# Kernel optimization log

Measured on AMD Instinct MI355X. Metric: run time of the kernel, lower is better.

The kernel has to match this reference:

```python
import jax, jax.numpy as jnp
import numpy as np

N = 100000           # nodes
E = 1600000          # directed edges (avg degree 16)
G = 64               # graphs in batch


def gcn_conv(x, src, dst, ew, W, b, n):
    """PyG GCNConv with edge weights and self-loops already appended.

    out[i] = sum_{(j->i)} d[j]^-1/2 * ew * d[i]^-1/2 * (x W)[j] + b
    where d[i] = sum of incoming edge weights at i (incl. self-loop).
    """
    xw = x @ W                                               # [n, out]
    deg = jax.ops.segment_sum(ew, dst, num_segments=n)       # [n]
    dinv = jnp.where(deg > 0, jax.lax.rsqrt(deg), 0.0)
    norm = dinv[src] * ew * dinv[dst]                        # [e]
    msg = xw[src] * norm[:, None]                            # [e, out] gather
    out = jax.ops.segment_sum(msg, dst, num_segments=n)      # scatter-add
    return out + b


def setup_inputs() -> dict:
    key = jax.random.key(0)
    ks = jax.random.split(key, 10)
    x = jax.random.normal(ks[0], (N, 256), dtype=jnp.float32)
    edge_index = jax.random.randint(ks[1], (2, E), 0, N, dtype=jnp.int64)
    edge_weight = jax.random.uniform(ks[2], (E,), dtype=jnp.float32)
    batch = jnp.sort(jax.random.randint(ks[3], (N,), 0, G, dtype=jnp.int64))
    s = 0.05
    W1 = jax.random.normal(ks[4], (256, 128), dtype=jnp.float32) * s
    b1 = jnp.zeros((128,), dtype=jnp.float32)
    W2 = jax.random.normal(ks[5], (128, 64), dtype=jnp.float32) * s
    b2 = jnp.zeros((64,), dtype=jnp.float32)
    Wfc = jax.random.normal(ks[6], (64, 1), dtype=jnp.float32) * s
    bfc = jnp.zeros((1,), dtype=jnp.float32)
    return {"x": x, "edge_index": edge_index, "edge_weight": edge_weight,
            "batch": batch, "W1": W1, "b1": b1, "W2": W2, "b2": b2,
            "Wfc": Wfc, "bfc": bfc}


def reference(x, edge_index, edge_weight, batch, W1, b1, W2, b2, Wfc, bfc):
    n = x.shape[0]
    loop = jnp.arange(n, dtype=edge_index.dtype)
    src = jnp.concatenate([edge_index[0], loop])             # add self-loops
    dst = jnp.concatenate([edge_index[1], loop])
    ew = jnp.concatenate([edge_weight, jnp.ones((n,), x.dtype)])

    h = jax.nn.relu(gcn_conv(x, src, dst, ew, W1, b1, n))    # [N,128]
    h = jax.nn.relu(gcn_conv(h, src, dst, ew, W2, b2, n))    # [N,64]

    # global_mean_pool over batch ids
    sums = jax.ops.segment_sum(h, batch, num_segments=G)     # [G,64]
    cnt = jax.ops.segment_sum(jnp.ones((n,), h.dtype), batch, num_segments=G)
    pooled = sums / jnp.maximum(cnt, 1.0)[:, None]
    return pooled @ Wfc + bfc                                # [G,1]
```

## Files before the change

kernel.cpp:

```cpp
#include <hip/hip_runtime.h>
#include <hip/hip_bf16.h>
#include <hip/hip_fp16.h>
#include <hip/hip_fp8.h>


static inline int ceil_div_ll(long long a, int b) { return (int)((a + b - 1) / b); }

typedef __attribute__((ext_vector_type(8))) short bf16x8;
typedef __attribute__((ext_vector_type(4))) float f32x4;

#define FIX_SCALE 33554432.0f

__device__ inline unsigned short f2bf(float f) {
    __hip_bfloat16 h = __float2bfloat16(f);
    return *reinterpret_cast<unsigned short*>(&h);
}
__device__ inline float bf2f(unsigned short u) {
    unsigned int x = ((unsigned int)u) << 16;
    return __uint_as_float(x);
}
__device__ inline unsigned char f32_to_fp8(float f) {
    return __hip_cvt_float_to_fp8(f, __HIP_SATFINITE, __HIP_E4M3);
}
__device__ inline float fp8_to_f32(unsigned int v) {
    unsigned int s = v >> 7;
    unsigned int e = (v >> 3) & 15;
    unsigned int m = v & 7;
    float r;
    if (e) r = __uint_as_float(((e + 120) << 23) | (m << 20));
    else   r = (float)m * 0.001953125f;
    return s ? -r : r;
}

__global__ void k_init_pk(unsigned long long* __restrict__ pk, int n) {
    int i = blockIdx.x * blockDim.x + threadIdx.x;
    if (i < n) pk[i] = (unsigned long long)(1u << 25);
}

__global__ void k_deg_count(const int* __restrict__ dst, const float* __restrict__ ew,
                            unsigned long long* __restrict__ pk, int* __restrict__ slot, int E) {
    int t = blockIdx.x * blockDim.x + threadIdx.x;
    int e = t * 4;
    if (e + 4 <= E) {
        int4   d4 = *(const int4*)(dst + e);
        float4 w4 = *(const float4*)(ew + e);
        unsigned long long o0 = atomicAdd(&pk[d4.x],
            (1ull << 32) | (unsigned long long)__float2uint_rn(w4.x * FIX_SCALE));
        unsigned long long o1 = atomicAdd(&pk[d4.y],
            (1ull << 32) | (unsigned long long)__float2uint_rn(w4.y * FIX_SCALE));
        unsigned long long o2 = atomicAdd(&pk[d4.z],
            (1ull << 32) | (unsigned long long)__float2uint_rn(w4.z * FIX_SCALE));
        unsigned long long o3 = atomicAdd(&pk[d4.w],
            (1ull << 32) | (unsigned long long)__float2uint_rn(w4.w * FIX_SCALE));
        *(int4*)(slot + e) = make_int4((int)(o0 >> 32), (int)(o1 >> 32),
                                       (int)(o2 >> 32), (int)(o3 >> 32));
    } else if (e < E) {
        for (int k = e; k < E; ++k) {
            unsigned int fx = __float2uint_rn(ew[k] * FIX_SCALE);
            unsigned long long old =
                atomicAdd(&pk[dst[k]], (1ull << 32) | (unsigned long long)fx);
            slot[k] = (int)(old >> 32);
        }
    }
}

__global__ void k_finish(const unsigned long long* __restrict__ pk, float* __restrict__ dinv,
                         int* __restrict__ count, float* __restrict__ sums, int nsums, int n) {
    int i = blockIdx.x * blockDim.x + threadIdx.x;
    if (i < n) {
        unsigned long long v = pk[i];
        float deg = (float)(unsigned int)(v & 0xffffffffull) * (1.0f / FIX_SCALE);
        dinv[i] = (deg > 0.f) ? rsqrtf(deg) : 0.f;
        count[i] = (int)(v >> 32);
    }
    if (i < nsums) sums[i] = 0.0f;
}

constexpr int SC_T = 256;
constexpr int SC_PER = 16;
constexpr int SC_CHUNK = SC_T * SC_PER;

__global__ void k_scan_a(const int* __restrict__ count, int* __restrict__ bsum, int n) {
    __shared__ int lds[SC_T];
    int b = blockIdx.x, t = threadIdx.x;
    int base = b * SC_CHUNK + t * SC_PER;
    int s = 0;
#pragma unroll
    for (int k = 0; k < SC_PER; ++k) {
        int idx = base + k;
        if (idx < n) s += count[idx];
    }
    lds[t] = s;
    __syncthreads();
    for (int off = 128; off > 0; off >>= 1) {
        if (t < off) lds[t] += lds[t + off];
        __syncthreads();
    }
    if (t == 0) bsum[b] = lds[0];
}

__global__ void k_scan_b(int* __restrict__ bsum, int nb) {
    if (threadIdx.x == 0) {
        int run = 0;
        for (int i = 0; i < nb; ++i) { int c = bsum[i]; bsum[i] = run; run += c; }
    }
}

__global__ void k_scan_c(const int* __restrict__ count, int* __restrict__ rowptr,
                         const int* __restrict__ bsum, int n) {
    __shared__ int lds[SC_T];
    int b = blockIdx.x, t = threadIdx.x;
    int base = b * SC_CHUNK + t * SC_PER;
    int v[SC_PER];
    int s = 0;
#pragma unroll
    for (int k = 0; k < SC_PER; ++k) {
        int idx = base + k;
        v[k] = (idx < n) ? count[idx] : 0;
        s += v[k];
    }
    lds[t] = s;
    for (int off = 1; off < SC_T; off <<= 1) {
        __syncthreads();
        int tmp = (t >= off) ? lds[t - off] : 0;
        __syncthreads();
        lds[t] += tmp;
    }
    __syncthreads();
    int run = bsum[b] + lds[t] - s;
#pragma unroll
    for (int k = 0; k < SC_PER; ++k) {
        int idx = base + k;
        if (idx < n) {
            rowptr[idx] = run;
            run += v[k];
            if (idx == n - 1) rowptr[n] = run;
        }
    }
}

__global__ void k_csr_fill(const int* __restrict__ src, const int* __restrict__ dst,
                           const float* __restrict__ ew, const float* __restrict__ dinv,
                           const int* __restrict__ rowptr, const int* __restrict__ slot,
                           int2* __restrict__ csr, int E) {
    int e = blockIdx.x * blockDim.x + threadIdx.x;
    if (e < E) {
        int s = src[e], d = dst[e];
        int pos = rowptr[d] + slot[e];
        float coef = dinv[s] * ew[e] * dinv[d];
        csr[pos] = make_int2(s, __float_as_int(coef));
    }
}

template <int KDIM, int ODIM>
__global__ void k_wpack(const float* __restrict__ W, unsigned short* __restrict__ wpk) {
    constexpr int NKS = KDIM / 32, NF = ODIM / 16;
    int t = blockIdx.x * blockDim.x + threadIdx.x;
    if (t >= NKS * NF * 64) return;
    int lane = t & 63;
    int nf   = (t >> 6) % NF;
    int ks   = t / (64 * NF);
    int col  = nf * 16 + (lane & 15);
    int kb   = ks * 32 + (lane >> 4) * 8;
    bf16x8 hi, lo;
#pragma unroll
    for (int i = 0; i < 8; ++i) {
        float w = W[(size_t)(kb + i) * ODIM + col];
        unsigned short h = f2bf(w);
        hi[i] = (short)h;
        lo[i] = (short)f2bf(w - bf2f(h));
    }
    size_t base = (size_t)t * 8;
    *(bf16x8*)(wpk + base) = hi;
    *(bf16x8*)(wpk + (size_t)KDIM * ODIM + base) = lo;
}

template <int KDIM, int ODIM>
__global__ void k_gemm_mfma(const float* __restrict__ X,
                            const unsigned short* __restrict__ wpk,
                            unsigned char* __restrict__ Y, int n) {
    constexpr int NKS = KDIM / 32, NF = ODIM / 16;
    int wid  = threadIdx.x >> 6;
    int lane = threadIdx.x & 63;
    int rowbase = blockIdx.x * 64 + wid * 16;
    int arow = rowbase + (lane & 15);
    int kb0  = (lane >> 4) * 8;
    const unsigned short* wlo = wpk + (size_t)KDIM * ODIM;
    bool aok = (arow < n);
    const float* xr = X + (size_t)arow * KDIM + kb0;

    f32x4 acc[NF];
#pragma unroll
    for (int f = 0; f < NF; ++f) acc[f] = (f32x4){0.f, 0.f, 0.f, 0.f};

#pragma unroll
    for (int ks = 0; ks < NKS; ++ks) {
        f32x4 a0 = (f32x4){0.f, 0.f, 0.f, 0.f};
        f32x4 a1 = (f32x4){0.f, 0.f, 0.f, 0.f};
        if (aok) {
            a0 = *(const f32x4*)(xr + ks * 32);
            a1 = *(const f32x4*)(xr + ks * 32 + 4);
        }
        bf16x8 ahi, alo;
#pragma unroll
        for (int i = 0; i < 4; ++i) {
            unsigned short h0 = f2bf(a0[i]);
            ahi[i]     = (short)h0;
            alo[i]     = (short)f2bf(a0[i] - bf2f(h0));
            unsigned short h1 = f2bf(a1[i]);
            ahi[i + 4] = (short)h1;
            alo[i + 4] = (short)f2bf(a1[i] - bf2f(h1));
        }
#pragma unroll
        for (int f = 0; f < NF; ++f) {
            size_t fb = (((size_t)ks * NF + f) * 64 + lane) * 8;
            bf16x8 bhi = *(const bf16x8*)(wpk + fb);
            bf16x8 blo = *(const bf16x8*)(wlo + fb);
            acc[f] = __builtin_amdgcn_mfma_f32_16x16x32_bf16(ahi, bhi, acc[f], 0, 0, 0);
            acc[f] = __builtin_amdgcn_mfma_f32_16x16x32_bf16(alo, bhi, acc[f], 0, 0, 0);
            acc[f] = __builtin_amdgcn_mfma_f32_16x16x32_bf16(ahi, blo, acc[f], 0, 0, 0);
        }
    }

    int r0  = rowbase + (lane >> 4) * 4;
    int col = lane & 15;
#pragma unroll
    for (int f = 0; f < NF; ++f) {
#pragma unroll
        for (int i = 0; i < 4; ++i) {
            int r = r0 + i;
            if (r < n) Y[(size_t)r * ODIM + f * 16 + col] = f32_to_fp8(acc[f][i]);
        }
    }
}

template <int KDIM, int ODIM>
__global__ void k_gemm_mfma_bfA(const unsigned short* __restrict__ X,
                                const unsigned short* __restrict__ wpk,
                                unsigned short* __restrict__ Y, int n) {
    constexpr int NKS = KDIM / 32, NF = ODIM / 16;
    int wid  = threadIdx.x >> 6;
    int lane = threadIdx.x & 63;
    int rowbase = blockIdx.x * 64 + wid * 16;
    int arow = rowbase + (lane & 15);
    int kb0  = (lane >> 4) * 8;
    const unsigned short* wlo = wpk + (size_t)KDIM * ODIM;
    bool aok = (arow < n);
    const unsigned short* xr = X + (size_t)arow * KDIM + kb0;

    f32x4 acc[NF];
#pragma unroll
    for (int f = 0; f < NF; ++f) acc[f] = (f32x4){0.f, 0.f, 0.f, 0.f};

#pragma unroll
    for (int ks = 0; ks < NKS; ++ks) {
        bf16x8 a = (bf16x8){0, 0, 0, 0, 0, 0, 0, 0};
        if (aok) a = *(const bf16x8*)(xr + ks * 32);
#pragma unroll
        for (int f = 0; f < NF; ++f) {
            size_t fb = (((size_t)ks * NF + f) * 64 + lane) * 8;
            bf16x8 bhi = *(const bf16x8*)(wpk + fb);
            bf16x8 blo = *(const bf16x8*)(wlo + fb);
            acc[f] = __builtin_amdgcn_mfma_f32_16x16x32_bf16(a, bhi, acc[f], 0, 0, 0);
            acc[f] = __builtin_amdgcn_mfma_f32_16x16x32_bf16(a, blo, acc[f], 0, 0, 0);
        }
    }

    int r0  = rowbase + (lane >> 4) * 4;
    int col = lane & 15;
#pragma unroll
    for (int f = 0; f < NF; ++f) {
#pragma unroll
        for (int i = 0; i < 4; ++i) {
            int r = r0 + i;
            if (r < n) Y[(size_t)r * ODIM + f * 16 + col] = f2bf(acc[f][i]);
        }
    }
}

__global__ __launch_bounds__(256, 2)
void k_gather1(const unsigned char* __restrict__ xw, const int* __restrict__ rowptr,
               const int2* __restrict__ csr,
               const float* __restrict__ dinv, const float* __restrict__ bias,
               unsigned short* __restrict__ out, int n) {
    int wave = threadIdx.x >> 6;
    int lane = threadIdx.x & 63;
    int i = blockIdx.x * 4 + wave;
    if (i >= n) return;

    float dv = dinv[i];
    float sl = dv * dv;
    int e0 = __builtin_amdgcn_readfirstlane(rowptr[i]);
    int e1 = __builtin_amdgcn_readfirstlane(rowptr[i + 1]);

    const unsigned short* base = (const unsigned short*)xw;
    unsigned int su = base[(size_t)i * 64 + lane];
    float ax0 = fp8_to_f32(su & 0xff) * sl;
    float ay0 = fp8_to_f32(su >> 8) * sl;
    float ax1 = 0.f, ay1 = 0.f, ax2 = 0.f, ay2 = 0.f, ax3 = 0.f, ay3 = 0.f;
    int e = e0;
    for (; e + 8 <= e1; e += 8) {
        int2 p0 = csr[e + 0], p1 = csr[e + 1], p2 = csr[e + 2], p3 = csr[e + 3];
        int2 p4 = csr[e + 4], p5 = csr[e + 5], p6 = csr[e + 6], p7 = csr[e + 7];
        unsigned int u0 = base[(size_t)p0.x * 64 + lane];
        unsigned int u1 = base[(size_t)p1.x * 64 + lane];
        unsigned int u2 = base[(size_t)p2.x * 64 + lane];
        unsigned int u3 = base[(size_t)p3.x * 64 + lane];
        unsigned int u4 = base[(size_t)p4.x * 64 + lane];
        unsigned int u5 = base[(size_t)p5.x * 64 + lane];
        unsigned int u6 = base[(size_t)p6.x * 64 + lane];
        unsigned int u7 = base[(size_t)p7.x * 64 + lane];
        float c0 = __int_as_float(p0.y), c1 = __int_as_float(p1.y);
        float c2 = __int_as_float(p2.y), c3 = __int_as_float(p3.y);
        float c4 = __int_as_float(p4.y), c5 = __int_as_float(p5.y);
        float c6 = __int_as_float(p6.y), c7 = __int_as_float(p7.y);
        ax0 += c0 * fp8_to_f32(u0 & 0xff); ay0 += c0 * fp8_to_f32(u0 >> 8);
        ax1 += c1 * fp8_to_f32(u1 & 0xff); ay1 += c1 * fp8_to_f32(u1 >> 8);
        ax2 += c2 * fp8_to_f32(u2 & 0xff); ay2 += c2 * fp8_to_f32(u2 >> 8);
        ax3 += c3 * fp8_to_f32(u3 & 0xff); ay3 += c3 * fp8_to_f32(u3 >> 8);
        ax0 += c4 * fp8_to_f32(u4 & 0xff); ay0 += c4 * fp8_to_f32(u4 >> 8);
        ax1 += c5 * fp8_to_f32(u5 & 0xff); ay1 += c5 * fp8_to_f32(u5 >> 8);
        ax2 += c6 * fp8_to_f32(u6 & 0xff); ay2 += c6 * fp8_to_f32(u6 >> 8);
        ax3 += c7 * fp8_to_f32(u7 & 0xff); ay3 += c7 * fp8_to_f32(u7 >> 8);
    }
    for (; e + 2 <= e1; e += 2) {
        int2 p0 = csr[e + 0], p1 = csr[e + 1];
        unsigned int u0 = base[(size_t)p0.x * 64 + lane];
        unsigned int u1 = base[(size_t)p1.x * 64 + lane];
        float c0 = __int_as_float(p0.y), c1 = __int_as_float(p1.y);
        ax0 += c0 * fp8_to_f32(u0 & 0xff); ay0 += c0 * fp8_to_f32(u0 >> 8);
        ax1 += c1 * fp8_to_f32(u1 & 0xff); ay1 += c1 * fp8_to_f32(u1 >> 8);
    }
    if (e < e1) {
        int2 p0 = csr[e];
        unsigned int u0 = base[(size_t)p0.x * 64 + lane];
        float c0 = __int_as_float(p0.y);
        ax0 += c0 * fp8_to_f32(u0 & 0xff); ay0 += c0 * fp8_to_f32(u0 >> 8);
    }
    float2 bb = *((const float2*)bias + lane);
    float rx = fmaxf((ax0 + ax1) + (ax2 + ax3) + bb.x, 0.f);
    float ry = fmaxf((ay0 + ay1) + (ay2 + ay3) + bb.y, 0.f);
    unsigned int packed = (unsigned int)f2bf(rx) | ((unsigned int)f2bf(ry) << 16);
    ((unsigned int*)(out + (size_t)i * 128))[lane] = packed;
}

__global__ __launch_bounds__(256, 2)
void k_gather2_pool(const unsigned short* __restrict__ xw, const int* __restrict__ rowptr,
                    const int2* __restrict__ csr,
                    const float* __restrict__ dinv, const float* __restrict__ bias,
                    const int* __restrict__ batch, float* __restrict__ sums, int n) {
    constexpr int NPW = 4;
    int gwave = (blockIdx.x * blockDim.x + threadIdx.x) >> 6;
    int lane = threadIdx.x & 63;
    int i0 = gwave * NPW;
    if (i0 >= n) return;
    int i1 = min(i0 + NPW, n);

    float bb = bias[lane];
    float acc = 0.f;
    int cg = __builtin_amdgcn_readfirstlane(batch[i0]);

    for (int i = i0; i < i1; ++i) {
        int g = __builtin_amdgcn_readfirstlane(batch[i]);
        if (g != cg) {
            atomicAdd(&sums[cg * 64 + lane], acc);
            acc = 0.f;
            cg = g;
        }
        float dv = dinv[i];
        float sl = dv * dv;
        int e0 = __builtin_amdgcn_readfirstlane(rowptr[i]);
        int e1 = __builtin_amdgcn_readfirstlane(rowptr[i + 1]);

        float a0 = bf2f(xw[(size_t)i * 64 + lane]) * sl;
        float a1 = 0.f, a2 = 0.f, a3 = 0.f;
        int e = e0;
        for (; e + 8 <= e1; e += 8) {
            int2 p0 = csr[e + 0], p1 = csr[e + 1], p2 = csr[e + 2], p3 = csr[e + 3];
            int2 p4 = csr[e + 4], p5 = csr[e + 5], p6 = csr[e + 6], p7 = csr[e + 7];
            float v0 = bf2f(xw[(size_t)p0.x * 64 + lane]);
            float v1 = bf2f(xw[(size_t)p1.x * 64 + lane]);
            float v2 = bf2f(xw[(size_t)p2.x * 64 + lane]);
            float v3 = bf2f(xw[(size_t)p3.x * 64 + lane]);
            float v4 = bf2f(xw[(size_t)p4.x * 64 + lane]);
            float v5 = bf2f(xw[(size_t)p5.x * 64 + lane]);
            float v6 = bf2f(xw[(size_t)p6.x * 64 + lane]);
            float v7 = bf2f(xw[(size_t)p7.x * 64 + lane]);
            a0 += __int_as_float(p0.y) * v0; a1 += __int_as_float(p1.y) * v1;
            a2 += __int_as_float(p2.y) * v2; a3 += __int_as_float(p3.y) * v3;
            a0 += __int_as_float(p4.y) * v4; a1 += __int_as_float(p5.y) * v5;
            a2 += __int_as_float(p6.y) * v6; a3 += __int_as_float(p7.y) * v7;
        }
        for (; e + 2 <= e1; e += 2) {
            int2 p0 = csr[e + 0], p1 = csr[e + 1];
            a0 += __int_as_float(p0.y) * bf2f(xw[(size_t)p0.x * 64 + lane]);
            a1 += __int_as_float(p1.y) * bf2f(xw[(size_t)p1.x * 64 + lane]);
        }
        if (e < e1) {
            int2 p0 = csr[e];
            a0 += __int_as_float(p0.y) * bf2f(xw[(size_t)p0.x * 64 + lane]);
        }
        acc += fmaxf((a0 + a1) + (a2 + a3) + bb, 0.f);
    }
    atomicAdd(&sums[cg * 64 + lane], acc);
}

__global__ void k_head(const float* __restrict__ sums, const int* __restrict__ batch,
                       const float* __restrict__ Wfc, const float* __restrict__ bfc,
                       float* __restrict__ out, int n) {
    int g = blockIdx.x;
    int f = threadIdx.x;
    int lo0 = 0, hi0 = n;
    while (lo0 < hi0) { int m = (lo0 + hi0) >> 1; if (batch[m] < g) lo0 = m + 1; else hi0 = m; }
    int lo1 = lo0, hi1 = n;
    while (lo1 < hi1) { int m = (lo1 + hi1) >> 1; if (batch[m] < g + 1) lo1 = m + 1; else hi1 = m; }
    float cnt = (float)(lo1 - lo0);
    float v = sums[g * 64 + f] * Wfc[f];
#pragma unroll
    for (int o = 32; o > 0; o >>= 1) v += __shfl_down(v, o);
    if (f == 0) out[g] = v / fmaxf(cnt, 1.0f) + bfc[0];
}

extern "C" void kernel_launch(void* const* d_in, const int* in_sizes, int n_in,
                              void* d_out, int out_size, void* d_ws, size_t ws_size,
                              hipStream_t stream) {
    const float* x    = (const float*)d_in[0];
    const int*   ei   = (const int*)d_in[1];
    const float* ew   = (const float*)d_in[2];
    const int*   bat  = (const int*)d_in[3];
    const float* W1   = (const float*)d_in[4];
    const float* b1   = (const float*)d_in[5];
    const float* W2   = (const float*)d_in[6];
    const float* b2   = (const float*)d_in[7];
    const float* Wfc  = (const float*)d_in[8];
    const float* bfc  = (const float*)d_in[9];
    float*       out  = (float*)d_out;

    const int N = in_sizes[0] / 256;
    const int E = in_sizes[2];
    const int G = out_size;

    const int* src = ei;
    const int* dst = ei + E;

    const int NB_SCAN = (N + SC_CHUNK - 1) / SC_CHUNK;

    const int Npad = (N + 4) & ~3;
    unsigned long long* pk     = (unsigned long long*)d_ws;
    float*              dinv   = (float*)(pk + Npad);
    int*                count  = (int*)(dinv + Npad);
    int*                rowptr = count + Npad;
    int*                bsum   = rowptr + Npad;
    int*                slot   = bsum + ((NB_SCAN + 4) & ~3);
    int2*               csr    = (int2*)(slot + ((E + 4) & ~3));
    unsigned short*     wpk1   = (unsigned short*)(csr + E);
    unsigned short*     wpk2   = wpk1 + 2 * 256 * 128;
    float*              sums   = (float*)(wpk2 + 2 * 128 * 64);
    unsigned char*      bufA   = (unsigned char*)(sums + ((G * 64 + 4) & ~3));
    unsigned short*     bufH1  = (unsigned short*)(bufA + (size_t)N * 128);

    const int B = 256;

    k_init_pk<<<ceil_div_ll(N, B), B, 0, stream>>>(pk, N);
    k_deg_count<<<ceil_div_ll((E + 3) / 4, B), B, 0, stream>>>(dst, ew, pk, slot, E);
    k_finish<<<ceil_div_ll(N, B), B, 0, stream>>>(pk, dinv, count, sums, G * 64, N);

    k_scan_a<<<NB_SCAN, SC_T, 0, stream>>>(count, bsum, N);
    k_scan_b<<<1, 64, 0, stream>>>(bsum, NB_SCAN);
    k_scan_c<<<NB_SCAN, SC_T, 0, stream>>>(count, rowptr, bsum, N);
    k_csr_fill<<<ceil_div_ll(E, B), B, 0, stream>>>(src, dst, ew, dinv, rowptr,
                                                    slot, csr, E);

    k_wpack<256, 128><<<(8 * 8 * 64 + B - 1) / B, B, 0, stream>>>(W1, wpk1);
    k_wpack<128, 64><<<(4 * 4 * 64 + B - 1) / B, B, 0, stream>>>(W2, wpk2);

    k_gemm_mfma<256, 128><<<ceil_div_ll(N, 64), 256, 0, stream>>>(x, wpk1, bufA, N);
    k_gather1<<<ceil_div_ll(N, 4), 256, 0, stream>>>(
        bufA, rowptr, csr, dinv, b1, bufH1, N);

    k_gemm_mfma_bfA<128, 64><<<ceil_div_ll(N, 64), 256, 0, stream>>>(
        bufH1, wpk2, (unsigned short*)bufA, N);
    {
        int waves = ceil_div_ll(N, 4);
        int blocks = ceil_div_ll(waves, 4);
        k_gather2_pool<<<blocks, 256, 0, stream>>>(
            (const unsigned short*)bufA, rowptr, csr, dinv, b2, bat, sums, N);
    }

    k_head<<<G, 64, 0, stream>>>(sums, bat, Wfc, bfc, out, N);
}
```

Measured before the change: 359.2 us.

## Split each wave into two half-waves gathering different edges with wider loads

Both gather kernels now have each half of a 64-lane wave handle alternate edges. Each lane loads 4 bytes per neighbor row instead of 2, so one wave-wide load fetches two neighbor rows. The halves' partial sums are combined with a cross-half shuffle before bias, ReLU and output. This is meant to issue fewer, wider memory instructions per edge. The cost is extra shuffles, extra select logic for the odd-edge tail, and more per-lane conversion work.

```diff
diff --git a/kernel.cpp b/kernel.cpp
--- a/kernel.cpp
+++ b/kernel.cpp
@@ -15,9 +15,8 @@
     __hip_bfloat16 h = __float2bfloat16(f);
     return *reinterpret_cast<unsigned short*>(&h);
 }
-__device__ inline float bf2f(unsigned short u) {
-    unsigned int x = ((unsigned int)u) << 16;
-    return __uint_as_float(x);
+__device__ inline float bf2f(unsigned int u) {
+    return __uint_as_float((u & 0xffffu) << 16);
 }
 __device__ inline unsigned char f32_to_fp8(float f) {
     return __hip_cvt_float_to_fp8(f, __HIP_SATFINITE, __HIP_E4M3);
@@ -285,6 +284,8 @@
                unsigned short* __restrict__ out, int n) {
     int wave = threadIdx.x >> 6;
     int lane = threadIdx.x & 63;
+    int half = lane >> 5;
+    int hl   = lane & 31;
     int i = blockIdx.x * 4 + wave;
     if (i >= n) return;
 
@@ -293,55 +294,60 @@
     int e0 = __builtin_amdgcn_readfirstlane(rowptr[i]);
     int e1 = __builtin_amdgcn_readfirstlane(rowptr[i + 1]);
 
-    const unsigned short* base = (const unsigned short*)xw;
-    unsigned int su = base[(size_t)i * 64 + lane];
-    float ax0 = fp8_to_f32(su & 0xff) * sl;
-    float ay0 = fp8_to_f32(su >> 8) * sl;
-    float ax1 = 0.f, ay1 = 0.f, ax2 = 0.f, ay2 = 0.f, ax3 = 0.f, ay3 = 0.f;
+    unsigned int su = *(const unsigned int*)(xw + (size_t)i * 128 + hl * 4);
+    float s0 = fp8_to_f32(su & 0xff) * sl;
+    float s1 = fp8_to_f32((su >> 8) & 0xff) * sl;
+    float s2 = fp8_to_f32((su >> 16) & 0xff) * sl;
+    float s3 = fp8_to_f32(su >> 24) * sl;
+
+    float ac0 = 0.f, ac1 = 0.f, ac2 = 0.f, ac3 = 0.f;
     int e = e0;
     for (; e + 8 <= e1; e += 8) {
-        int2 p0 = csr[e + 0], p1 = csr[e + 1], p2 = csr[e + 2], p3 = csr[e + 3];
-        int2 p4 = csr[e + 4], p5 = csr[e + 5], p6 = csr[e + 6], p7 = csr[e + 7];
-        unsigned int u0 = base[(size_t)p0.x * 64 + lane];
-        unsigned int u1 = base[(size_t)p1.x * 64 + lane];
-        unsigned int u2 = base[(size_t)p2.x * 64 + lane];
-        unsigned int u3 = base[(size_t)p3.x * 64 + lane];
-        unsigned int u4 = base[(size_t)p4.x * 64 + lane];
-        unsigned int u5 = base[(size_t)p5.x * 64 + lane];
-        unsigned int u6 = base[(size_t)p6.x * 64 + lane];
-        unsigned int u7 = base[(size_t)p7.x * 64 + lane];
-        float c0 = __int_as_float(p0.y), c1 = __int_as_float(p1.y);
-        float c2 = __int_as_float(p2.y), c3 = __int_as_float(p3.y);
-        float c4 = __int_as_float(p4.y), c5 = __int_as_float(p5.y);
-        float c6 = __int_as_float(p6.y), c7 = __int_as_float(p7.y);
-        ax0 += c0 * fp8_to_f32(u0 & 0xff); ay0 += c0 * fp8_to_f32(u0 >> 8);
-        ax1 += c1 * fp8_to_f32(u1 & 0xff); ay1 += c1 * fp8_to_f32(u1 >> 8);
-        ax2 += c2 * fp8_to_f32(u2 & 0xff); ay2 += c2 * fp8_to_f32(u2 >> 8);
-        ax3 += c3 * fp8_to_f32(u3 & 0xff); ay3 += c3 * fp8_to_f32(u3 >> 8);
-        ax0 += c4 * fp8_to_f32(u4 & 0xff); ay0 += c4 * fp8_to_f32(u4 >> 8);
-        ax1 += c5 * fp8_to_f32(u5 & 0xff); ay1 += c5 * fp8_to_f32(u5 >> 8);
-        ax2 += c6 * fp8_to_f32(u6 & 0xff); ay2 += c6 * fp8_to_f32(u6 >> 8);
-        ax3 += c7 * fp8_to_f32(u7 & 0xff); ay3 += c7 * fp8_to_f32(u7 >> 8);
+        int2 q0 = csr[e + 0 + half];
+        int2 q1 = csr[e + 2 + half];
+        int2 q2 = csr[e + 4 + half];
+        int2 q3 = csr[e + 6 + half];
+        unsigned int u0 = *(const unsigned int*)(xw + (size_t)q0.x * 128 + hl * 4);
+        unsigned int u1 = *(const unsigned int*)(xw + (size_t)q1.x * 128 + hl * 4);
+        unsigned int u2 = *(const unsigned int*)(xw + (size_t)q2.x * 128 + hl * 4);
+        unsigned int u3 = *(const unsigned int*)(xw + (size_t)q3.x * 128 + hl * 4);
+        float c0 = __int_as_float(q0.y), c1 = __int_as_float(q1.y);
+        float c2 = __int_as_float(q2.y), c3 = __int_as_float(q3.y);
+        ac0 += c0 * fp8_to_f32(u0 & 0xff);         ac1 += c0 * fp8_to_f32((u0 >> 8) & 0xff);
+        ac2 += c0 * fp8_to_f32((u0 >> 16) & 0xff); ac3 += c0 * fp8_to_f32(u0 >> 24);
+        ac0 += c1 * fp8_to_f32(u1 & 0xff);         ac1 += c1 * fp8_to_f32((u1 >> 8) & 0xff);
+        ac2 += c1 * fp8_to_f32((u1 >> 16) & 0xff); ac3 += c1 * fp8_to_f32(u1 >> 24);
+        ac0 += c2 * fp8_to_f32(u2 & 0xff);         ac1 += c2 * fp8_to_f32((u2 >> 8) & 0xff);
+        ac2 += c2 * fp8_to_f32((u2 >> 16) & 0xff); ac3 += c2 * fp8_to_f32(u2 >> 24);
+        ac0 += c3 * fp8_to_f32(u3 & 0xff);         ac1 += c3 * fp8_to_f32((u3 >> 8) & 0xff);
+        ac2 += c3 * fp8_to_f32((u3 >> 16) & 0xff); ac3 += c3 * fp8_to_f32(u3 >> 24);
     }
     for (; e + 2 <= e1; e += 2) {
-        int2 p0 = csr[e + 0], p1 = csr[e + 1];
-        unsigned int u0 = base[(size_t)p0.x * 64 + lane];
-        unsigned int u1 = base[(size_t)p1.x * 64 + lane];
-        float c0 = __int_as_float(p0.y), c1 = __int_as_float(p1.y);
-        ax0 += c0 * fp8_to_f32(u0 & 0xff); ay0 += c0 * fp8_to_f32(u0 >> 8);
-        ax1 += c1 * fp8_to_f32(u1 & 0xff); ay1 += c1 * fp8_to_f32(u1 >> 8);
+        int2 q = csr[e + half];
+        unsigned int u = *(const unsigned int*)(xw + (size_t)q.x * 128 + hl * 4);
+        float c = __int_as_float(q.y);
+        ac0 += c * fp8_to_f32(u & 0xff);         ac1 += c * fp8_to_f32((u >> 8) & 0xff);
+        ac2 += c * fp8_to_f32((u >> 16) & 0xff); ac3 += c * fp8_to_f32(u >> 24);
     }
     if (e < e1) {
-        int2 p0 = csr[e];
-        unsigned int u0 = base[(size_t)p0.x * 64 + lane];
-        float c0 = __int_as_float(p0.y);
-        ax0 += c0 * fp8_to_f32(u0 & 0xff); ay0 += c0 * fp8_to_f32(u0 >> 8);
-    }
-    float2 bb = *((const float2*)bias + lane);
-    float rx = fmaxf((ax0 + ax1) + (ax2 + ax3) + bb.x, 0.f);
-    float ry = fmaxf((ay0 + ay1) + (ay2 + ay3) + bb.y, 0.f);
-    unsigned int packed = (unsigned int)f2bf(rx) | ((unsigned int)f2bf(ry) << 16);
-    ((unsigned int*)(out + (size_t)i * 128))[lane] = packed;
+        int2 q = csr[e];
+        unsigned int u = *(const unsigned int*)(xw + (size_t)q.x * 128 + hl * 4);
+        float c = half ? 0.f : __int_as_float(q.y);
+        ac0 += c * fp8_to_f32(u & 0xff);         ac1 += c * fp8_to_f32((u >> 8) & 0xff);
+        ac2 += c * fp8_to_f32((u >> 16) & 0xff); ac3 += c * fp8_to_f32(u >> 24);
+    }
+    ac0 += __shfl_xor(ac0, 32);
+    ac1 += __shfl_xor(ac1, 32);
+    ac2 += __shfl_xor(ac2, 32);
+    ac3 += __shfl_xor(ac3, 32);
+    float4 bb = ((const float4*)bias)[hl];
+    float f0 = fmaxf(ac0 + s0 + bb.x, 0.f);
+    float f1 = fmaxf(ac1 + s1 + bb.y, 0.f);
+    float f2 = fmaxf(ac2 + s2 + bb.z, 0.f);
+    float f3 = fmaxf(ac3 + s3 + bb.w, 0.f);
+    unsigned int w = half ? ((unsigned int)f2bf(f2) | ((unsigned int)f2bf(f3) << 16))
+                          : ((unsigned int)f2bf(f0) | ((unsigned int)f2bf(f1) << 16));
+    ((unsigned int*)(out + (size_t)i * 128))[2 * hl + half] = w;
 }
 
 __global__ __launch_bounds__(256, 2)
@@ -352,19 +358,22 @@
     constexpr int NPW = 4;
     int gwave = (blockIdx.x * blockDim.x + threadIdx.x) >> 6;
     int lane = threadIdx.x & 63;
+    int half = lane >> 5;
+    int hl   = lane & 31;
     int i0 = gwave * NPW;
     if (i0 >= n) return;
     int i1 = min(i0 + NPW, n);
 
-    float bb = bias[lane];
-    float acc = 0.f;
+    float2 bb = ((const float2*)bias)[hl];
+    float p0 = 0.f, p1 = 0.f;
     int cg = __builtin_amdgcn_readfirstlane(batch[i0]);
 
     for (int i = i0; i < i1; ++i) {
         int g = __builtin_amdgcn_readfirstlane(batch[i]);
         if (g != cg) {
-            atomicAdd(&sums[cg * 64 + lane], acc);
-            acc = 0.f;
+            float pv = half ? p1 : p0;
+            atomicAdd(&sums[cg * 64 + 2 * hl + half], pv);
+            p0 = 0.f; p1 = 0.f;
             cg = g;
         }
         float dv = dinv[i];
@@ -372,37 +381,46 @@
         int e0 = __builtin_amdgcn_readfirstlane(rowptr[i]);
         int e1 = __builtin_amdgcn_readfirstlane(rowptr[i + 1]);
 
-        float a0 = bf2f(xw[(size_t)i * 64 + lane]) * sl;
-        float a1 = 0.f, a2 = 0.f, a3 = 0.f;
+        unsigned int su = ((const unsigned int*)(xw + (size_t)i * 64))[hl];
+        float s0 = bf2f(su) * sl;
+        float s1 = bf2f(su >> 16) * sl;
+        float a0 = 0.f, a1 = 0.f;
         int e = e0;
         for (; e + 8 <= e1; e += 8) {
-            int2 p0 = csr[e + 0], p1 = csr[e + 1], p2 = csr[e + 2], p3 = csr[e + 3];
-            int2 p4 = csr[e + 4], p5 = csr[e + 5], p6 = csr[e + 6], p7 = csr[e + 7];
-            float v0 = bf2f(xw[(size_t)p0.x * 64 + lane]);
-            float v1 = bf2f(xw[(size_t)p1.x * 64 + lane]);
-            float v2 = bf2f(xw[(size_t)p2.x * 64 + lane]);
-            float v3 = bf2f(xw[(size_t)p3.x * 64 + lane]);
-            float v4 = bf2f(xw[(size_t)p4.x * 64 + lane]);
-            float v5 = bf2f(xw[(size_t)p5.x * 64 + lane]);
-            float v6 = bf2f(xw[(size_t)p6.x * 64 + lane]);
-            float v7 = bf2f(xw[(size_t)p7.x * 64 + lane]);
-            a0 += __int_as_float(p0.y) * v0; a1 += __int_as_float(p1.y) * v1;
-            a2 += __int_as_float(p2.y) * v2; a3 += __int_as_float(p3.y) * v3;
-            a0 += __int_as_float(p4.y) * v4; a1 += __int_as_float(p5.y) * v5;
-            a2 += __int_as_float(p6.y) * v6; a3 += __int_as_float(p7.y) * v7;
+            int2 q0 = csr[e + 0 + half];
+            int2 q1 = csr[e + 2 + half];
+            int2 q2 = csr[e + 4 + half];
+            int2 q3 = csr[e + 6 + half];
+            unsigned int u0 = ((const unsigned int*)(xw + (size_t)q0.x * 64))[hl];
+            unsigned int u1 = ((const unsigned int*)(xw + (size_t)q1.x * 64))[hl];
+            unsigned int u2 = ((const unsigned int*)(xw + (size_t)q2.x * 64))[hl];
+            unsigned int u3 = ((const unsigned int*)(xw + (size_t)q3.x * 64))[hl];
+            float c0 = __int_as_float(q0.y), c1 = __int_as_float(q1.y);
+            float c2 = __int_as_float(q2.y), c3 = __int_as_float(q3.y);
+            a0 += c0 * bf2f(u0); a1 += c0 * bf2f(u0 >> 16);
+            a0 += c1 * bf2f(u1); a1 += c1 * bf2f(u1 >> 16);
+            a0 += c2 * bf2f(u2); a1 += c2 * bf2f(u2 >> 16);
+            a0 += c3 * bf2f(u3); a1 += c3 * bf2f(u3 >> 16);
         }
         for (; e + 2 <= e1; e += 2) {
-            int2 p0 = csr[e + 0], p1 = csr[e + 1];
-            a0 += __int_as_float(p0.y) * bf2f(xw[(size_t)p0.x * 64 + lane]);
-            a1 += __int_as_float(p1.y) * bf2f(xw[(size_t)p1.x * 64 + lane]);
+            int2 q = csr[e + half];
+            unsigned int u = ((const unsigned int*)(xw + (size_t)q.x * 64))[hl];
+            float c = __int_as_float(q.y);
+            a0 += c * bf2f(u); a1 += c * bf2f(u >> 16);
         }
         if (e < e1) {
-            int2 p0 = csr[e];
-            a0 += __int_as_float(p0.y) * bf2f(xw[(size_t)p0.x * 64 + lane]);
-        }
-        acc += fmaxf((a0 + a1) + (a2 + a3) + bb, 0.f);
-    }
-    atomicAdd(&sums[cg * 64 + lane], acc);
+            int2 q = csr[e];
+            unsigned int u = ((const unsigned int*)(xw + (size_t)q.x * 64))[hl];
+            float c = half ? 0.f : __int_as_float(q.y);
+            a0 += c * bf2f(u); a1 += c * bf2f(u >> 16);
+        }
+        a0 += __shfl_xor(a0, 32);
+        a1 += __shfl_xor(a1, 32);
+        p0 += fmaxf(a0 + s0 + bb.x, 0.f);
+        p1 += fmaxf(a1 + s1 + bb.y, 0.f);
+    }
+    float pv = half ? p1 : p0;
+    atomicAdd(&sums[cg * 64 + 2 * hl + half], pv);
 }
 
 __global__ void k_head(const float* __restrict__ sums, const int* __restrict__ batch,
```

Result: slower. 380.8 us (+6.0%).
